# Optimization experiments

Hardware: AMD Instinct MI355X
Metric: run time of the kernel (lower is better)

## Reference

```python
import jax, jax.numpy as jnp
from jax import lax
import numpy as np

IMG = 224
NB = IMG // 8  # 28 blocks per spatial dim

# DCT-II (ortho) 8x8 basis matrix
_D = np.cos(np.pi * (2 * np.arange(8)[None, :] + 1) * np.arange(8)[:, None] / 16.0) * np.sqrt(2.0 / 8.0)
_D[0, :] *= 1.0 / np.sqrt(2.0)
DCT8 = jnp.asarray(_D, dtype=jnp.float32)


def _conv(x, w, b, s):
    y = lax.conv_general_dilated(x, w, (s, s), 'SAME', dimension_numbers=('NCHW', 'OIHW', 'NCHW'))
    return y + b[None, :, None, None]


def _pool7(h):  # adaptive avg pool 56x56 -> 7x7, flatten
    B = h.shape[0]
    return h.reshape(B, 64, 7, 8, 7, 8).mean(axis=(3, 5)).reshape(B, -1)


def setup_inputs() -> dict:
    key = jax.random.key(0)
    ks = jax.random.split(key, 16)
    r = jax.nn.initializers.normal(0.02)
    inp = {
        'x': jax.random.uniform(ks[0], (64, 3, IMG, IMG), jnp.float32),
        'w_stem': r(ks[1], (64, 3, 7, 7), jnp.float32), 'b_stem': jnp.zeros((64,), jnp.float32),
        'w1': r(ks[2], (128, 64, 3, 3), jnp.float32), 'b1': jnp.zeros((128,), jnp.float32),
        'w2': r(ks[3], (256, 128, 3, 3), jnp.float32), 'b2': jnp.zeros((256,), jnp.float32),
        'w3': r(ks[4], (512, 256, 3, 3), jnp.float32), 'b3': jnp.zeros((512,), jnp.float32),
        'wd1': r(ks[5], (32, 3, 3, 3), jnp.float32), 'bd1': jnp.zeros((32,), jnp.float32),
        'wd2': r(ks[6], (64, 32, 3, 3), jnp.float32), 'bd2': jnp.zeros((64,), jnp.float32),
        'wf1': r(ks[7], (32, 6, 3, 3), jnp.float32), 'bf1': jnp.zeros((32,), jnp.float32),
        'wf2': r(ks[8], (64, 32, 3, 3), jnp.float32), 'bf2': jnp.zeros((64,), jnp.float32),
        'W_freq': r(ks[9], (6272, 512), jnp.float32), 'b_freq': jnp.zeros((512,), jnp.float32),
        'W_fu1': r(ks[10], (1024, 1024), jnp.float32), 'b_fu1': jnp.zeros((1024,), jnp.float32),
        'W_fu2': r(ks[11], (1024, 512), jnp.float32), 'b_fu2': jnp.zeros((512,), jnp.float32),
        'W_cls': r(ks[12], (512, 2), jnp.float32), 'b_cls': jnp.zeros((2,), jnp.float32),
        'temp': 1.5 * jnp.ones((1,), jnp.float32),
    }
    return inp


def reference(x, w_stem, b_stem, w1, b1, w2, b2, w3, b3, wd1, bd1, wd2, bd2,
              wf1, bf1, wf2, bf2, W_freq, b_freq, W_fu1, b_fu1, W_fu2, b_fu2,
              W_cls, b_cls, temp):
    relu = jax.nn.relu
    B = x.shape[0]
    # --- CNN backbone (resnet18 surrogate): 4 stride-2 stages -> GAP 512 ---
    h = relu(_conv(x, w_stem, b_stem, 2))
    h = relu(_conv(h, w1, b1, 2))
    h = relu(_conv(h, w2, b2, 2))
    h = relu(_conv(h, w3, b3, 2))
    backbone_feat = h.mean(axis=(2, 3))  # [B, 512]
    # --- DCT branch: grayscale -> batched 8x8 block DCT-II ortho -> mean -> resize ---
    gray = (0.299 * x[:, 0] + 0.587 * x[:, 1] + 0.114 * x[:, 2]) * 255.0  # [B,224,224]
    blocks = gray.reshape(B, NB, 8, NB, 8).transpose(0, 1, 3, 2, 4)  # [B,28,28,8,8]
    dctb = jnp.einsum('ij,bmnjk,lk->bmnil', DCT8, blocks, DCT8)  # D @ blk @ D^T
    dct_img = dctb.mean(axis=(1, 2))  # [B,8,8]
    dct_img = jax.image.resize(dct_img, (B, IMG, IMG), 'bilinear')
    dct_in = jnp.broadcast_to(dct_img[:, None], (B, 3, IMG, IMG))
    hd = relu(_conv(dct_in, wd1, bd1, 2))
    hd = relu(_conv(hd, wd2, bd2, 2))  # [B,64,56,56]
    dct_pooled = _pool7(hd)  # [B,3136]
    # --- FFT branch: batched 2D FFT, interleaved real/imag per channel -> 6 ch ---
    f = jnp.fft.fft2(x)  # [B,3,224,224] complex
    fft_in = jnp.stack([f.real, f.imag], axis=2).reshape(B, 6, IMG, IMG).astype(x.dtype)
    hf = relu(_conv(fft_in, wf1, bf1, 2))
    hf = relu(_conv(hf, wf2, bf2, 2))
    fft_pooled = _pool7(hf)  # [B,3136]
    # --- fusion + classifier + temperature scaling ---
    freq = relu(jnp.concatenate([dct_pooled, fft_pooled], axis=1) @ W_freq + b_freq)
    comb = jnp.concatenate([backbone_feat, freq], axis=1)  # [B,1024]
    fused = relu(relu(comb @ W_fu1 + b_fu1) @ W_fu2 + b_fu2)
    logits = fused @ W_cls + b_cls
    calibrated = logits / temp
    return (logits, calibrated)
```

## Files before the change

kernel.cpp:

```cpp
#include <hip/hip_runtime.h>

#ifndef M_PI
#define M_PI 3.14159265358979323846
#endif


#define BATCH 64

typedef __bf16 bf16x8 __attribute__((ext_vector_type(8)));
typedef float f32x4 __attribute__((ext_vector_type(4)));

__device__ __forceinline__ unsigned short f2bf(float f) {
    unsigned u = __float_as_uint(f);
    u += 0x7FFF + ((u >> 16) & 1);
    return (unsigned short)(u >> 16);
}
__device__ __forceinline__ unsigned packsplit(float v) {
    unsigned short h = f2bf(v);
    float hf = __uint_as_float(((unsigned)h) << 16);
    unsigned short l = f2bf(v - hf);
    return (((unsigned)h) << 16) | (unsigned)l;
}

union U8frag { bf16x8 v; unsigned d[4]; };

__device__ __forceinline__ void unpack8(const unsigned* p, bf16x8& hi, bf16x8& lo) {
    uint4 a = *(const uint4*)p;
    uint4 b = *(const uint4*)(p + 4);
    U8frag H, L;
    H.d[0] = __builtin_amdgcn_perm(a.y, a.x, 0x07060302u);
    L.d[0] = __builtin_amdgcn_perm(a.y, a.x, 0x05040100u);
    H.d[1] = __builtin_amdgcn_perm(a.w, a.z, 0x07060302u);
    L.d[1] = __builtin_amdgcn_perm(a.w, a.z, 0x05040100u);
    H.d[2] = __builtin_amdgcn_perm(b.y, b.x, 0x07060302u);
    L.d[2] = __builtin_amdgcn_perm(b.y, b.x, 0x05040100u);
    H.d[3] = __builtin_amdgcn_perm(b.w, b.z, 0x07060302u);
    L.d[3] = __builtin_amdgcn_perm(b.w, b.z, 0x05040100u);
    hi = H.v; lo = L.v;
}

__device__ __forceinline__ bf16x8 bfneg(bf16x8 v) {
    U8frag a; a.v = v;
    a.d[0] ^= 0x80008000u; a.d[1] ^= 0x80008000u;
    a.d[2] ^= 0x80008000u; a.d[3] ^= 0x80008000u;
    return a.v;
}

__global__ void prep_w(const float* __restrict__ w, unsigned* __restrict__ dst,
                       int Co, int Ci) {
    int idx = blockIdx.x * 256 + threadIdx.x;
    int tot = Co * Ci * 9;
    if (idx >= tot) return;
    int k9 = idx % 9;
    int rest = idx / 9;
    int ci = rest % Ci, co = rest / Ci;
    dst[((size_t)k9 * Co + co) * Ci + ci] = packsplit(w[idx]);
}

__global__ void pack_f32(const float* __restrict__ src, unsigned* __restrict__ dst, int n) {
    int i = blockIdx.x * 256 + threadIdx.x;
    if (i < n) dst[i] = packsplit(src[i]);
}

__global__ __launch_bounds__(256)
void conv3x3s2_mfma(const unsigned* __restrict__ inP, const unsigned* __restrict__ wP,
                    const float* __restrict__ bias,
                    unsigned* __restrict__ outPk, float* __restrict__ outF0,
                    float* __restrict__ outF1,
                    int Ci, int Co, int Hin, int Win, int Hout, int Wout,
                    int NTOT, int ciPer, int mode) {
    __shared__ unsigned sA[128 * 36];
    __shared__ unsigned sB[64 * 36];
    const int tid = threadIdx.x;
    const int wv = tid >> 6, lane = tid & 63;
    const int ciBeg = blockIdx.z * ciPer;
    const int coT0 = blockIdx.y * 128;
    const int HWin = Hin * Win, HWout = Hout * Wout;

    const int nG = blockIdx.x * 64 + (tid >> 2);
    const int kqB = tid & 3;
    int bb = 0, yy = 0, xx = 0;
    bool nval = nG < NTOT;
    if (nval) {
        bb = nG / HWout;
        int rem = nG - bb * HWout;
        yy = rem / Wout;
        xx = rem - yy * Wout;
    }
    const unsigned baseImg = (unsigned)bb * Ci * HWin;
    const int coA = tid >> 1, halfA = tid & 1;

    f32x4 acc[2][4];
#pragma unroll
    for (int s = 0; s < 2; s++)
#pragma unroll
        for (int t = 0; t < 4; t++) acc[s][t] = (f32x4){0.f, 0.f, 0.f, 0.f};

    for (int k9 = 0; k9 < 9; k9++) {
        int ky = k9 / 3, kx = k9 - ky * 3;
        int iy = 2 * yy + ky, ix = 2 * xx + kx;
        bool bval = nval && iy < Hin && ix < Win;
        unsigned off0 = baseImg + (unsigned)iy * Win + (unsigned)ix;
        const unsigned* wbase = wP + ((size_t)k9 * Co + coT0 + coA) * Ci + ciBeg + halfA * 16;

        for (int c0 = 0; c0 < ciPer; c0 += 32) {
            __syncthreads();
            {
                const uint4* g = (const uint4*)(wbase + c0);
                uint4 v0 = g[0], v1 = g[1], v2 = g[2], v3 = g[3];
                uint4* d = (uint4*)(sA + coA * 36 + halfA * 16);
                d[0] = v0; d[1] = v1; d[2] = v2; d[3] = v3;
            }
            {
                unsigned u[8];
                const unsigned cbase = off0 + (unsigned)(ciBeg + c0 + kqB * 8) * HWin;
#pragma unroll
                for (int j = 0; j < 8; j++)
                    u[j] = bval ? inP[cbase + (unsigned)j * HWin] : 0u;
                uint4* d = (uint4*)(sB + (tid >> 2) * 36 + kqB * 8);
                uint4 w0; w0.x = u[0]; w0.y = u[1]; w0.z = u[2]; w0.w = u[3];
                uint4 w1; w1.x = u[4]; w1.y = u[5]; w1.z = u[6]; w1.w = u[7];
                d[0] = w0; d[1] = w1;
            }
            __syncthreads();

            bf16x8 ah[2], al[2], bh[4], bl[4];
            const int m = lane & 15, q = lane >> 4;
#pragma unroll
            for (int s = 0; s < 2; s++)
                unpack8(sA + (wv * 32 + s * 16 + m) * 36 + q * 8, ah[s], al[s]);
#pragma unroll
            for (int t = 0; t < 4; t++)
                unpack8(sB + (t * 16 + m) * 36 + q * 8, bh[t], bl[t]);

#pragma unroll
            for (int s = 0; s < 2; s++)
#pragma unroll
                for (int t = 0; t < 4; t++)
                    acc[s][t] = __builtin_amdgcn_mfma_f32_16x16x32_bf16(ah[s], bh[t], acc[s][t], 0, 0, 0);
#pragma unroll
            for (int s = 0; s < 2; s++)
#pragma unroll
                for (int t = 0; t < 4; t++)
                    acc[s][t] = __builtin_amdgcn_mfma_f32_16x16x32_bf16(ah[s], bl[t], acc[s][t], 0, 0, 0);
#pragma unroll
            for (int s = 0; s < 2; s++)
#pragma unroll
                for (int t = 0; t < 4; t++)
                    acc[s][t] = __builtin_amdgcn_mfma_f32_16x16x32_bf16(al[s], bh[t], acc[s][t], 0, 0, 0);
        }
    }

    const int m = lane & 15, q = lane >> 4;
#pragma unroll
    for (int t = 0; t < 4; t++) {
        int n_g = blockIdx.x * 64 + t * 16 + m;
        if (n_g >= NTOT) continue;
        int b = n_g / HWout;
        int rem = n_g - b * HWout;
        size_t nb = (size_t)b * Co * HWout + rem;
#pragma unroll
        for (int s = 0; s < 2; s++) {
            int co_l = wv * 32 + s * 16 + q * 4;
#pragma unroll
            for (int r = 0; r < 4; r++) {
                int co_g = coT0 + co_l + r;
                float v = acc[s][t][r];
                size_t addr = nb + (size_t)co_g * HWout;
                if (mode == 0) {
                    v += bias[co_g];
                    v = v > 0.f ? v : 0.f;
                    outPk[addr] = packsplit(v);
                } else {
                    (blockIdx.z == 0 ? outF0 : outF1)[addr] = v;
                }
            }
        }
    }
}

__global__ __launch_bounds__(256)
void conv3x3s2_mfma64(const unsigned* __restrict__ inP, const unsigned* __restrict__ wP,
                      const float* __restrict__ bias, float* __restrict__ outF,
                      int Hin, int Win, int Hout, int Wout, int NTOT) {
    const int Ci = 32;
    __shared__ unsigned sA[64 * 36];
    __shared__ unsigned sB[64 * 36];
    const int tid = threadIdx.x;
    const int wv = tid >> 6, lane = tid & 63;
    const int HWin = Hin * Win, HWout = Hout * Wout;

    const int nG = blockIdx.x * 64 + (tid >> 2);
    const int kq = tid & 3;
    int bb = 0, yy = 0, xx = 0;
    bool nval = nG < NTOT;
    if (nval) {
        bb = nG / HWout;
        int rem = nG - bb * HWout;
        yy = rem / Wout;
        xx = rem - yy * Wout;
    }
    const unsigned baseImg = (unsigned)bb * Ci * HWin;
    const int ch = wv & 1, nh = wv >> 1;

    f32x4 acc[2][2];
#pragma unroll
    for (int s = 0; s < 2; s++)
#pragma unroll
        for (int t = 0; t < 2; t++) acc[s][t] = (f32x4){0.f, 0.f, 0.f, 0.f};

    for (int k9 = 0; k9 < 9; k9++) {
        int ky = k9 / 3, kx = k9 - ky * 3;
        int iy = 2 * yy + ky, ix = 2 * xx + kx;
        bool bval = nval && iy < Hin && ix < Win;
        unsigned off0 = baseImg + (unsigned)iy * Win + (unsigned)ix;
        __syncthreads();
        {
            const unsigned* g = wP + ((size_t)k9 * 64 + (tid >> 2)) * Ci + kq * 8;
            uint4 v0 = *(const uint4*)g;
            uint4 v1 = *(const uint4*)(g + 4);
            uint4* d = (uint4*)(sA + (tid >> 2) * 36 + kq * 8);
            d[0] = v0; d[1] = v1;
        }
        {
            unsigned u[8];
            const unsigned cbase = off0 + (unsigned)(kq * 8) * HWin;
#pragma unroll
            for (int j = 0; j < 8; j++)
                u[j] = bval ? inP[cbase + (unsigned)j * HWin] : 0u;
            uint4* d = (uint4*)(sB + (tid >> 2) * 36 + kq * 8);
            uint4 w0; w0.x = u[0]; w0.y = u[1]; w0.z = u[2]; w0.w = u[3];
            uint4 w1; w1.x = u[4]; w1.y = u[5]; w1.z = u[6]; w1.w = u[7];
            d[0] = w0; d[1] = w1;
        }
        __syncthreads();

        bf16x8 ah[2], al[2], bh[2], bl[2];
        const int m = lane & 15, q = lane >> 4;
#pragma unroll
        for (int s = 0; s < 2; s++)
            unpack8(sA + (ch * 32 + s * 16 + m) * 36 + q * 8, ah[s], al[s]);
#pragma unroll
        for (int t = 0; t < 2; t++)
            unpack8(sB + (nh * 32 + t * 16 + m) * 36 + q * 8, bh[t], bl[t]);

#pragma unroll
        for (int s = 0; s < 2; s++)
#pragma unroll
            for (int t = 0; t < 2; t++)
                acc[s][t] = __builtin_amdgcn_mfma_f32_16x16x32_bf16(ah[s], bh[t], acc[s][t], 0, 0, 0);
#pragma unroll
        for (int s = 0; s < 2; s++)
#pragma unroll
            for (int t = 0; t < 2; t++)
                acc[s][t] = __builtin_amdgcn_mfma_f32_16x16x32_bf16(ah[s], bl[t], acc[s][t], 0, 0, 0);
#pragma unroll
        for (int s = 0; s < 2; s++)
#pragma unroll
            for (int t = 0; t < 2; t++)
                acc[s][t] = __builtin_amdgcn_mfma_f32_16x16x32_bf16(al[s], bh[t], acc[s][t], 0, 0, 0);
    }

    const int m = lane & 15, q = lane >> 4;
#pragma unroll
    for (int t = 0; t < 2; t++) {
        int n_g = blockIdx.x * 64 + nh * 32 + t * 16 + m;
        if (n_g >= NTOT) continue;
        int b = n_g / HWout;
        int rem = n_g - b * HWout;
        size_t nb = (size_t)b * 64 * HWout + rem;
#pragma unroll
        for (int s = 0; s < 2; s++) {
            int co0 = ch * 32 + s * 16 + q * 4;
#pragma unroll
            for (int r = 0; r < 4; r++) {
                int co = co0 + r;
                float v = acc[s][t][r] + bias[co];
                outF[nb + (size_t)co * HWout] = v > 0.f ? v : 0.f;
            }
        }
    }
}

__global__ void make_dft(unsigned* __restrict__ wre, unsigned* __restrict__ wim) {
    int idx = blockIdx.x * 256 + threadIdx.x;
    if (idx >= 224 * 224) return;
    int j = idx / 224, k = idx % 224;
    int m = (j * k) % 224;
    double a = -2.0 * M_PI * (double)m / 224.0;
    wre[idx] = packsplit((float)cos(a));
    wim[idx] = packsplit((float)sin(a));
}

__global__ void make_wsum(const float* __restrict__ wd1, float* __restrict__ wsum) {
    int idx = threadIdx.x;
    if (idx >= 288) return;
    int o = idx / 9, k = idx % 9;
    wsum[idx] = wd1[o * 27 + k] + wd1[o * 27 + 9 + k] + wd1[o * 27 + 18 + k];
}

__global__ __launch_bounds__(64)
void dft_mfma_s1(const unsigned* __restrict__ wre, const unsigned* __restrict__ wim,
                 const unsigned* __restrict__ xpk,
                 unsigned* __restrict__ ttre, unsigned* __restrict__ ttim) {
    const int z = blockIdx.z;
    const int m0 = blockIdx.x * 32, n0 = blockIdx.y * 32;
    const int lane = threadIdx.x;
    const int ml = lane & 15, q = lane >> 4;
    const unsigned* xb = xpk + (size_t)z * 50176;

    f32x4 cre[2][2], cim[2][2];
#pragma unroll
    for (int s = 0; s < 2; s++)
#pragma unroll
        for (int t = 0; t < 2; t++) { cre[s][t] = (f32x4){0,0,0,0}; cim[s][t] = (f32x4){0,0,0,0}; }

    for (int k0 = 0; k0 < 224; k0 += 32) {
        bf16x8 arh[2], arl[2], aih[2], ail[2], bh[2], bl[2];
#pragma unroll
        for (int s = 0; s < 2; s++) {
            int row = m0 + s * 16 + ml;
            unpack8(wre + row * 224 + k0 + q * 8, arh[s], arl[s]);
            unpack8(wim + row * 224 + k0 + q * 8, aih[s], ail[s]);
        }
#pragma unroll
        for (int t = 0; t < 2; t++)
            unpack8(xb + (n0 + t * 16 + ml) * 224 + k0 + q * 8, bh[t], bl[t]);

#pragma unroll
        for (int s = 0; s < 2; s++)
#pragma unroll
            for (int t = 0; t < 2; t++) {
                cre[s][t] = __builtin_amdgcn_mfma_f32_16x16x32_bf16(arh[s], bh[t], cre[s][t], 0, 0, 0);
                cre[s][t] = __builtin_amdgcn_mfma_f32_16x16x32_bf16(arh[s], bl[t], cre[s][t], 0, 0, 0);
                cre[s][t] = __builtin_amdgcn_mfma_f32_16x16x32_bf16(arl[s], bh[t], cre[s][t], 0, 0, 0);
                cim[s][t] = __builtin_amdgcn_mfma_f32_16x16x32_bf16(aih[s], bh[t], cim[s][t], 0, 0, 0);
                cim[s][t] = __builtin_amdgcn_mfma_f32_16x16x32_bf16(aih[s], bl[t], cim[s][t], 0, 0, 0);
                cim[s][t] = __builtin_amdgcn_mfma_f32_16x16x32_bf16(ail[s], bh[t], cim[s][t], 0, 0, 0);
            }
    }

    unsigned* tre = ttre + (size_t)z * 50176;
    unsigned* tim = ttim + (size_t)z * 50176;
#pragma unroll
    for (int s = 0; s < 2; s++)
#pragma unroll
        for (int t = 0; t < 2; t++)
#pragma unroll
            for (int r = 0; r < 4; r++) {
                int m = m0 + s * 16 + q * 4 + r;
                int n = n0 + t * 16 + ml;
                tre[m * 224 + n] = packsplit(cre[s][t][r]);
                tim[m * 224 + n] = packsplit(cim[s][t][r]);
            }
}

__global__ __launch_bounds__(64)
void dft_mfma_s2(const unsigned* __restrict__ wre, const unsigned* __restrict__ wim,
                 const unsigned* __restrict__ ttre, const unsigned* __restrict__ ttim,
                 float* __restrict__ fft_in) {
    const int z = blockIdx.z;
    const int m0 = blockIdx.x * 32, n0 = blockIdx.y * 32;
    const int lane = threadIdx.x;
    const int ml = lane & 15, q = lane >> 4;
    const unsigned* tre = ttre + (size_t)z * 50176;
    const unsigned* tim = ttim + (size_t)z * 50176;

    f32x4 cre[2][2], cim[2][2];
#pragma unroll
    for (int s = 0; s < 2; s++)
#pragma unroll
        for (int t = 0; t < 2; t++) { cre[s][t] = (f32x4){0,0,0,0}; cim[s][t] = (f32x4){0,0,0,0}; }

    for (int k0 = 0; k0 < 224; k0 += 32) {
        bf16x8 arh[2], arl[2], aih[2], ail[2];
        bf16x8 brh[2], brl[2], bih[2], bil[2];
#pragma unroll
        for (int s = 0; s < 2; s++) {
            int row = m0 + s * 16 + ml;
            unpack8(wre + row * 224 + k0 + q * 8, arh[s], arl[s]);
            unpack8(wim + row * 224 + k0 + q * 8, aih[s], ail[s]);
        }
#pragma unroll
        for (int t = 0; t < 2; t++) {
            int row = n0 + t * 16 + ml;
            unpack8(tre + row * 224 + k0 + q * 8, brh[t], brl[t]);
            unpack8(tim + row * 224 + k0 + q * 8, bih[t], bil[t]);
        }

#pragma unroll
        for (int t = 0; t < 2; t++) {
            bf16x8 nih = bfneg(bih[t]);
            bf16x8 nil = bfneg(bil[t]);
#pragma unroll
            for (int s = 0; s < 2; s++) {
                cre[s][t] = __builtin_amdgcn_mfma_f32_16x16x32_bf16(arh[s], brh[t], cre[s][t], 0, 0, 0);
                cre[s][t] = __builtin_amdgcn_mfma_f32_16x16x32_bf16(arh[s], brl[t], cre[s][t], 0, 0, 0);
                cre[s][t] = __builtin_amdgcn_mfma_f32_16x16x32_bf16(arl[s], brh[t], cre[s][t], 0, 0, 0);
                cre[s][t] = __builtin_amdgcn_mfma_f32_16x16x32_bf16(aih[s], nih, cre[s][t], 0, 0, 0);
                cre[s][t] = __builtin_amdgcn_mfma_f32_16x16x32_bf16(aih[s], nil, cre[s][t], 0, 0, 0);
                cre[s][t] = __builtin_amdgcn_mfma_f32_16x16x32_bf16(ail[s], nih, cre[s][t], 0, 0, 0);
                cim[s][t] = __builtin_amdgcn_mfma_f32_16x16x32_bf16(arh[s], bih[t], cim[s][t], 0, 0, 0);
                cim[s][t] = __builtin_amdgcn_mfma_f32_16x16x32_bf16(arh[s], bil[t], cim[s][t], 0, 0, 0);
                cim[s][t] = __builtin_amdgcn_mfma_f32_16x16x32_bf16(arl[s], bih[t], cim[s][t], 0, 0, 0);
                cim[s][t] = __builtin_amdgcn_mfma_f32_16x16x32_bf16(aih[s], brh[t], cim[s][t], 0, 0, 0);
                cim[s][t] = __builtin_amdgcn_mfma_f32_16x16x32_bf16(aih[s], brl[t], cim[s][t], 0, 0, 0);
                cim[s][t] = __builtin_amdgcn_mfma_f32_16x16x32_bf16(ail[s], brh[t], cim[s][t], 0, 0, 0);
            }
        }
    }

    const int b_loc = z / 3, c = z % 3;
    float* yre = fft_in + (size_t)(b_loc * 6 + 2 * c) * 50176;
    float* yim = yre + 50176;
#pragma unroll
    for (int s = 0; s < 2; s++)
#pragma unroll
        for (int t = 0; t < 2; t++)
#pragma unroll
            for (int r = 0; r < 4; r++) {
                int m = m0 + s * 16 + q * 4 + r;
                int n = n0 + t * 16 + ml;
                yre[m * 224 + n] = cre[s][t][r];
                yim[m * 224 + n] = cim[s][t][r];
            }
}

template <int CO_BLK, int TH, int TW, int CI_CHUNK, bool PACK>
__global__ __launch_bounds__(CO_BLK * TH)
void conv3x3_s2(const float* __restrict__ in, const float* __restrict__ w,
                const float* __restrict__ bias, float* __restrict__ out,
                int Ci, int Co, int Hin, int Win, int Hout, int Wout) {
    constexpr int IN_H = 2 * TH + 1;
    constexpr int IN_W = 2 * TW + 1;
    constexpr int IN_WP = 32;
    constexpr int WSTR = (CI_CHUNK * 9) | 1;
    __shared__ __align__(16) float s_in[CI_CHUNK][IN_H][IN_WP];
    __shared__ float s_w[CO_BLK * WSTR];

    const int tid = threadIdx.x;
    const int tiles_x = Wout / TW;
    const int tile = blockIdx.x;
    const int ty0 = (tile / tiles_x) * TH;
    const int tx0 = (tile % tiles_x) * TW;
    const int cog = blockIdx.y;
    const int b = blockIdx.z;
    const int co = tid % CO_BLK;
    const int ty = tid / CO_BLK;
    const int co_g = cog * CO_BLK + co;

    float acc[TW];
#pragma unroll
    for (int i = 0; i < TW; i++) acc[i] = 0.f;

    const float* in_b = in + (size_t)b * Ci * Hin * Win;
    const int iy0 = 2 * ty0, ix0 = 2 * tx0;

    for (int ci0 = 0; ci0 < Ci; ci0 += CI_CHUNK) {
        for (int idx = tid; idx < CI_CHUNK * IN_H * IN_W; idx += CO_BLK * TH) {
            int ci = idx / (IN_H * IN_W);
            int rem = idx % (IN_H * IN_W);
            int r = rem / IN_W, cc = rem % IN_W;
            int gy = iy0 + r, gx = ix0 + cc;
            float v = 0.f;
            if (gy < Hin && gx < Win)
                v = in_b[(size_t)(ci0 + ci) * Hin * Win + (size_t)gy * Win + gx];
            s_in[ci][r][cc] = v;
        }
        for (int idx = tid; idx < CO_BLK * CI_CHUNK * 9; idx += CO_BLK * TH) {
            int c = idx / (CI_CHUNK * 9);
            int k = idx % (CI_CHUNK * 9);
            s_w[c * WSTR + k] = w[((size_t)(cog * CO_BLK + c) * Ci + ci0) * 9 + k];
        }
        __syncthreads();

#pragma unroll
        for (int ci = 0; ci < CI_CHUNK; ci++) {
            float wr[9];
#pragma unroll
            for (int k = 0; k < 9; k++) wr[k] = s_w[co * WSTR + ci * 9 + k];
#pragma unroll
            for (int ky = 0; ky < 3; ky++) {
                float r[IN_WP];
                const float4* rowp = (const float4*)&s_in[ci][2 * ty + ky][0];
#pragma unroll
                for (int qq = 0; qq < IN_WP / 4; qq++) {
                    float4 v = rowp[qq];
                    r[4 * qq] = v.x; r[4 * qq + 1] = v.y; r[4 * qq + 2] = v.z; r[4 * qq + 3] = v.w;
                }
#pragma unroll
                for (int kx = 0; kx < 3; kx++) {
                    float wv = wr[ky * 3 + kx];
#pragma unroll
                    for (int xq = 0; xq < TW; xq++) acc[xq] += r[2 * xq + kx] * wv;
                }
            }
        }
        __syncthreads();
    }
    float bb = bias[co_g];
    size_t obase = ((size_t)b * Co + co_g) * Hout * Wout + (size_t)(ty0 + ty) * Wout + tx0;
#pragma unroll
    for (int xq = 0; xq < TW; xq++) {
        float v = acc[xq] + bb;
        v = v > 0.f ? v : 0.f;
        if (PACK)
            ((unsigned*)out)[obase + xq] = packsplit(v);
        else
            out[obase + xq] = v;
    }
}

__global__ __launch_bounds__(256)
void conv7x7_s2_pack(const float* __restrict__ in, const float* __restrict__ w,
                     const float* __restrict__ bias, unsigned* __restrict__ out) {
    constexpr int TH = 4, TW = 14;
    constexpr int IN_H = 13, IN_W = 33, IN_WP = 36, WSTR = 149;
    __shared__ __align__(16) float s_in[3][IN_H][IN_WP];
    __shared__ float s_w[64 * WSTR];
    const int tid = threadIdx.x;
    const int tile = blockIdx.x;
    const int tiles_x = 112 / TW;
    const int ty0 = (tile / tiles_x) * TH;
    const int tx0 = (tile % tiles_x) * TW;
    const int b = blockIdx.z;
    const int co = tid & 63;
    const int ty = tid >> 6;

    const float* in_b = in + (size_t)b * 3 * 224 * 224;
    const int iy0 = 2 * ty0 - 2, ix0 = 2 * tx0 - 2;

    for (int idx = tid; idx < 3 * IN_H * IN_W; idx += 256) {
        int ci = idx / (IN_H * IN_W);
        int rem = idx % (IN_H * IN_W);
        int r = rem / IN_W, cc = rem % IN_W;
        int gy = iy0 + r, gx = ix0 + cc;
        float v = 0.f;
        if (gy >= 0 && gy < 224 && gx >= 0 && gx < 224)
            v = in_b[(size_t)ci * 224 * 224 + (size_t)gy * 224 + gx];
        s_in[ci][r][cc] = v;
    }
    for (int idx = tid; idx < 64 * 147; idx += 256) {
        int c = idx / 147, k = idx % 147;
        s_w[c * WSTR + k] = w[c * 147 + k];
    }
    __syncthreads();

    float acc[TW];
#pragma unroll
    for (int i = 0; i < TW; i++) acc[i] = 0.f;

#pragma unroll
    for (int ci = 0; ci < 3; ci++) {
#pragma unroll
        for (int ky = 0; ky < 7; ky++) {
            float wr[7];
#pragma unroll
            for (int k = 0; k < 7; k++) wr[k] = s_w[co * WSTR + ci * 49 + ky * 7 + k];
            float r[IN_WP];
            const float4* rowp = (const float4*)&s_in[ci][2 * ty + ky][0];
#pragma unroll
            for (int qq = 0; qq < IN_WP / 4; qq++) {
                float4 v = rowp[qq];
                r[4 * qq] = v.x; r[4 * qq + 1] = v.y; r[4 * qq + 2] = v.z; r[4 * qq + 3] = v.w;
            }
#pragma unroll
            for (int kx = 0; kx < 7; kx++) {
                float wv = wr[kx];
#pragma unroll
                for (int xq = 0; xq < TW; xq++) acc[xq] += r[2 * xq + kx] * wv;
            }
        }
    }
    float bb = bias[co];
    unsigned* outp = out + ((size_t)b * 64 + co) * 112 * 112 + (size_t)(ty0 + ty) * 112 + tx0;
#pragma unroll
    for (int xq = 0; xq < TW; xq++) {
        float v = acc[xq] + bb;
        v = v > 0.f ? v : 0.f;
        outp[xq] = packsplit(v);
    }
}

__device__ __forceinline__ float dct_coef(int u, int i) {
    if (u == 0) return 0.35355339059327373f;
    return 0.5f * cosf((float)M_PI * (float)((2 * i + 1) * u) / 16.0f);
}

__global__ __launch_bounds__(256)
void dct_partial(const float* __restrict__ x, float* __restrict__ accum) {
    __shared__ float red[256];
    const int b = blockIdx.x, g = blockIdx.y;
    const int tid = threadIdx.x;
    const int ij = tid & 63;
    const int grp = tid >> 6;
    const int i = ij >> 3, j = ij & 7;
    const float* xb = x + (size_t)b * 3 * 50176;
    float s = 0.f;
    for (int blk = g * 4 + grp; blk < 784; blk += 48) {
        int m = blk / 28, n = blk % 28;
        size_t o = (size_t)(m * 8 + i) * 224 + n * 8 + j;
        s += 0.299f * xb[o] + 0.587f * xb[50176 + o] + 0.114f * xb[2 * 50176 + o];
    }
    red[tid] = s;
    __syncthreads();
    if (tid < 64)
        atomicAdd(&accum[b * 64 + tid],
                  red[tid] + red[tid + 64] + red[tid + 128] + red[tid + 192]);
}

__global__ __launch_bounds__(64)
void dct_final(const float* __restrict__ accum, float* __restrict__ dct_out) {
    __shared__ float Mb[64];
    const int b = blockIdx.x, tid = threadIdx.x;
    Mb[tid] = accum[b * 64 + tid] * (255.f / 784.f);
    __syncthreads();
    int u = tid >> 3, v = tid & 7;
    float acc = 0.f;
#pragma unroll
    for (int i2 = 0; i2 < 8; i2++) {
        float du = dct_coef(u, i2);
#pragma unroll
        for (int j2 = 0; j2 < 8; j2++) acc += du * Mb[i2 * 8 + j2] * dct_coef(v, j2);
    }
    dct_out[b * 64 + tid] = acc;
}

__global__ void resize_bilinear(const float* __restrict__ dct, float* __restrict__ out) {
    int idx = blockIdx.x * 256 + threadIdx.x;
    if (idx >= BATCH * 224 * 224) return;
    int b = idx / (224 * 224);
    int rem = idx % (224 * 224);
    int y = rem / 224, xx = rem % 224;
    float sy = fminf(fmaxf((y + 0.5f) * (1.f / 28.f) - 0.5f, 0.f), 7.f);
    float sx = fminf(fmaxf((xx + 0.5f) * (1.f / 28.f) - 0.5f, 0.f), 7.f);
    int y0 = (int)floorf(sy); if (y0 > 6) y0 = 6;
    int x0 = (int)floorf(sx); if (x0 > 6) x0 = 6;
    float ty = sy - y0, tx = sx - x0;
    const float* M = dct + b * 64;
    float v00 = M[y0 * 8 + x0], v01 = M[y0 * 8 + x0 + 1];
    float v10 = M[(y0 + 1) * 8 + x0], v11 = M[(y0 + 1) * 8 + x0 + 1];
    out[idx] = (1.f - ty) * ((1.f - tx) * v00 + tx * v01) + ty * ((1.f - tx) * v10 + tx * v11);
}

__global__ void pool7(const float* __restrict__ h, float* __restrict__ out,
                      int col_base, int n) {
    int idx = blockIdx.x * 256 + threadIdx.x;
    if (idx >= n) return;
    int b = idx / (64 * 49);
    int rem = idx % (64 * 49);
    int c = rem / 49;
    int ij = rem % 49;
    int i = ij / 7, j = ij % 7;
    const float* hp = h + ((size_t)(b * 64 + c)) * 56 * 56 + (size_t)i * 8 * 56 + j * 8;
    float s = 0.f;
#pragma unroll
    for (int r = 0; r < 8; r++)
#pragma unroll
        for (int q = 0; q < 8; q++) s += hp[r * 56 + q];
    out[(size_t)b * 6272 + col_base + c * 49 + ij] = s * (1.f / 64.f);
}

__global__ void gap2_kernel(const float* __restrict__ ha, const float* __restrict__ hb,
                            const float* __restrict__ bias, float* __restrict__ comb,
                            int nwaves) {
    int gt = blockIdx.x * blockDim.x + threadIdx.x;
    int wid = gt >> 6;
    int lane = gt & 63;
    if (wid >= nwaves) return;
    int b = wid / 512, c = wid % 512;
    const float* pa = ha + (size_t)wid * 196;
    const float* pb = hb + (size_t)wid * 196;
    float bbv = bias[c];
    float s = 0.f;
    for (int i = lane; i < 196; i += 64) {
        float v = pa[i] + pb[i] + bbv;
        s += v > 0.f ? v : 0.f;
    }
#pragma unroll
    for (int off = 32; off > 0; off >>= 1) s += __shfl_down(s, off);
    if (lane == 0) comb[(size_t)b * 1024 + c] = s * (1.f / 196.f);
}

__global__ __launch_bounds__(256)
void gemm64_atomic(const float* __restrict__ A, const float* __restrict__ Bm,
                   float* __restrict__ C, int N, int K, int KC) {
    __shared__ __align__(16) float sA[16][68];
    __shared__ __align__(16) float sB[16][68];
    const int tid = threadIdx.x;
    const int n0 = blockIdx.x * 64;
    const int kbase = blockIdx.z * KC;
    const int tr = (tid >> 4) << 2;
    const int tc = (tid & 15) << 2;
    float acc[4][4];
#pragma unroll
    for (int r = 0; r < 4; r++)
#pragma unroll
        for (int c = 0; c < 4; c++) acc[r][c] = 0.f;

    for (int k0 = 0; k0 < KC; k0 += 16) {
        for (int i = tid; i < 1024; i += 256) {
            int m = i >> 4, k = i & 15;
            sA[k][m] = A[(size_t)m * K + kbase + k0 + k];
        }
        for (int i = tid; i < 1024; i += 256) {
            int k = i >> 6, n = i & 63;
            sB[k][n] = Bm[(size_t)(kbase + k0 + k) * N + n0 + n];
        }
        __syncthreads();
#pragma unroll
        for (int k = 0; k < 16; k++) {
            float4 a = *(const float4*)&sA[k][tr];
            float4 bv = *(const float4*)&sB[k][tc];
            float av[4] = {a.x, a.y, a.z, a.w};
            float bb[4] = {bv.x, bv.y, bv.z, bv.w};
#pragma unroll
            for (int r = 0; r < 4; r++)
#pragma unroll
                for (int c = 0; c < 4; c++) acc[r][c] += av[r] * bb[c];
        }
        __syncthreads();
    }
#pragma unroll
    for (int r = 0; r < 4; r++)
#pragma unroll
        for (int c = 0; c < 4; c++)
            atomicAdd(&C[(size_t)(tr + r) * N + n0 + tc + c], acc[r][c]);
}

__global__ void bias_relu_copy(const float* __restrict__ src, const float* __restrict__ bias,
                               float* __restrict__ dst, int N, int dstStride, int dstOff) {
    int idx = blockIdx.x * 256 + threadIdx.x;
    if (idx >= BATCH * N) return;
    int b = idx / N, n = idx % N;
    float v = src[idx] + bias[n];
    dst[(size_t)b * dstStride + dstOff + n] = v > 0.f ? v : 0.f;
}

__global__ void logits_kernel(const float* __restrict__ fused, const float* __restrict__ Wc,
                              const float* __restrict__ bcls, const float* __restrict__ temp,
                              float* __restrict__ out) {
    int idx = threadIdx.x;
    if (idx >= 128) return;
    int b = idx >> 1, n = idx & 1;
    float s = bcls[n];
    const float* f = fused + (size_t)b * 512;
    for (int k = 0; k < 512; k++) s += f[k] * Wc[k * 2 + n];
    out[idx] = s;
    out[128 + idx] = s / temp[0];
}

extern "C" void kernel_launch(void* const* d_in, const int* in_sizes, int n_in,
                              void* d_out, int out_size, void* d_ws, size_t ws_size,
                              hipStream_t stream) {
    const float* x      = (const float*)d_in[0];
    const float* w_stem = (const float*)d_in[1];
    const float* b_stem = (const float*)d_in[2];
    const float* w1 = (const float*)d_in[3];   const float* b1 = (const float*)d_in[4];
    const float* w2 = (const float*)d_in[5];   const float* b2 = (const float*)d_in[6];
    const float* w3 = (const float*)d_in[7];   const float* b3 = (const float*)d_in[8];
    const float* wd1 = (const float*)d_in[9];  const float* bd1 = (const float*)d_in[10];
    const float* wd2 = (const float*)d_in[11]; const float* bd2 = (const float*)d_in[12];
    const float* wf1 = (const float*)d_in[13]; const float* bf1 = (const float*)d_in[14];
    const float* wf2 = (const float*)d_in[15]; const float* bf2 = (const float*)d_in[16];
    const float* W_freq = (const float*)d_in[17]; const float* b_freq = (const float*)d_in[18];
    const float* W_fu1  = (const float*)d_in[19]; const float* b_fu1  = (const float*)d_in[20];
    const float* W_fu2  = (const float*)d_in[21]; const float* b_fu2  = (const float*)d_in[22];
    const float* W_cls  = (const float*)d_in[23]; const float* b_cls  = (const float*)d_in[24];
    const float* temp   = (const float*)d_in[25];
    float* ws = (float*)d_ws;
    float* out = (float*)d_out;

    const size_t IMG2 = 224 * 224;

    size_t oWRE  = 0;
    size_t oWIM  = oWRE + IMG2;
    size_t oWSUM = oWIM + IMG2;
    size_t oDCT  = oWSUM + 288;
    size_t oDIMG = oDCT + (size_t)BATCH * 64;
    size_t oFREQIN  = oDIMG + (size_t)BATCH * IMG2;
    size_t oCOMB    = oFREQIN + (size_t)BATCH * 6272;
    size_t oFREQACC = oCOMB + (size_t)BATCH * 1024;
    size_t oFU1     = oFREQACC + (size_t)BATCH * 512;
    size_t oFUSED   = oFU1 + (size_t)BATCH * 1024;
    size_t oDCTACC  = oFUSED + (size_t)BATCH * 512;
    size_t oW1s     = oDCTACC + (size_t)BATCH * 64;
    size_t oW2s     = oW1s + 73728;
    size_t oW3s     = oW2s + 294912;
    size_t oWF2s    = oW3s + 1179648;
    size_t oWD2s    = oWF2s + 18432;
    size_t P        = oWD2s + 18432;

    int CB = 16;
    while (CB > 1 && (P + (size_t)CB * 1605632) * 4 > ws_size) CB >>= 1;
    size_t base   = P;
    size_t oSTEMP = base;
    size_t oC1P   = oSTEMP + (size_t)CB * 802816;
    size_t oC2P   = oC1P + (size_t)CB * 401408;
    size_t oC3a   = oC2P + (size_t)CB * 200704;
    size_t oC3b   = oC3a + (size_t)CB * 100352;
    size_t oXPK   = base;
    size_t oTTRE  = oXPK + (size_t)CB * 150528;
    size_t oTTIM  = oTTRE + (size_t)CB * 150528;
    size_t oFFTIN = oTTIM + (size_t)CB * 150528;
    size_t oBIG1  = oC1P;
    size_t oBIG2  = oC2P;

    unsigned* WREp = (unsigned*)(ws + oWRE);
    unsigned* WIMp = (unsigned*)(ws + oWIM);
    unsigned* W1s = (unsigned*)(ws + oW1s);
    unsigned* W2s = (unsigned*)(ws + oW2s);
    unsigned* W3s = (unsigned*)(ws + oW3s);
    unsigned* WF2s = (unsigned*)(ws + oWF2s);
    unsigned* WD2s = (unsigned*)(ws + oWD2s);
    unsigned* STEMP = (unsigned*)(ws + oSTEMP);
    unsigned* C1P   = (unsigned*)(ws + oC1P);
    unsigned* C2P   = (unsigned*)(ws + oC2P);
    unsigned* XPK   = (unsigned*)(ws + oXPK);
    unsigned* TTRE  = (unsigned*)(ws + oTTRE);
    unsigned* TTIM  = (unsigned*)(ws + oTTIM);
    unsigned* BIG1P = (unsigned*)(ws + oBIG1);

    hipMemsetAsync(ws + oFREQACC, 0,
                   (size_t)BATCH * (512 + 1024 + 512 + 64) * sizeof(float), stream);
    make_dft<<<196, 256, 0, stream>>>(WREp, WIMp);
    make_wsum<<<1, 288, 0, stream>>>(wd1, ws + oWSUM);
    prep_w<<<(128 * 64 * 9 + 255) / 256, 256, 0, stream>>>(w1, W1s, 128, 64);
    prep_w<<<(256 * 128 * 9 + 255) / 256, 256, 0, stream>>>(w2, W2s, 256, 128);
    prep_w<<<(512 * 256 * 9 + 255) / 256, 256, 0, stream>>>(w3, W3s, 512, 256);
    prep_w<<<(64 * 32 * 9 + 255) / 256, 256, 0, stream>>>(wf2, WF2s, 64, 32);
    prep_w<<<(64 * 32 * 9 + 255) / 256, 256, 0, stream>>>(wd2, WD2s, 64, 32);
    dct_partial<<<dim3(BATCH, 12), 256, 0, stream>>>(x, ws + oDCTACC);
    dct_final<<<BATCH, 64, 0, stream>>>(ws + oDCTACC, ws + oDCT);
    resize_bilinear<<<12544, 256, 0, stream>>>(ws + oDCT, ws + oDIMG);

    for (int b0 = 0; b0 < BATCH; b0 += CB) {
        const float* xc = x + (size_t)b0 * 3 * IMG2;
        pack_f32<<<(CB * 3 * (int)IMG2 + 255) / 256, 256, 0, stream>>>(
            xc, XPK, CB * 3 * (int)IMG2);
        dft_mfma_s1<<<dim3(7, 7, 3 * CB), 64, 0, stream>>>(WREp, WIMp, XPK, TTRE, TTIM);
        dft_mfma_s2<<<dim3(7, 7, 3 * CB), 64, 0, stream>>>(WREp, WIMp, TTRE, TTIM, ws + oFFTIN);
        conv3x3_s2<32, 8, 14, 6, true><<<dim3(112, 1, CB), 256, 0, stream>>>(
            ws + oFFTIN, wf1, bf1, ws + oBIG1, 6, 32, 224, 224, 112, 112);
        conv3x3s2_mfma64<<<dim3(CB * 3136 / 64, 1, 1), 256, 0, stream>>>(
            BIG1P, WF2s, bf2, ws + oBIG2, 112, 112, 56, 56, CB * 3136);
        pool7<<<(CB * 64 * 49 + 255) / 256, 256, 0, stream>>>(
            ws + oBIG2, ws + oFREQIN + (size_t)b0 * 6272, 3136, CB * 64 * 49);
        conv3x3_s2<32, 8, 14, 1, true><<<dim3(112, 1, CB), 256, 0, stream>>>(
            ws + oDIMG + (size_t)b0 * IMG2, ws + oWSUM, bd1, ws + oBIG1, 1, 32, 224, 224, 112, 112);
        conv3x3s2_mfma64<<<dim3(CB * 3136 / 64, 1, 1), 256, 0, stream>>>(
            BIG1P, WD2s, bd2, ws + oBIG2, 112, 112, 56, 56, CB * 3136);
        pool7<<<(CB * 64 * 49 + 255) / 256, 256, 0, stream>>>(
            ws + oBIG2, ws + oFREQIN + (size_t)b0 * 6272, 0, CB * 64 * 49);
        conv7x7_s2_pack<<<dim3(224, 1, CB), 256, 0, stream>>>(xc, w_stem, b_stem, STEMP);
        conv3x3s2_mfma<<<dim3((CB * 3136 + 63) / 64, 1, 1), 256, 0, stream>>>(
            STEMP, W1s, b1, C1P, nullptr, nullptr,
            64, 128, 112, 112, 56, 56, CB * 3136, 64, 0);
        conv3x3s2_mfma<<<dim3((CB * 784 + 63) / 64, 2, 1), 256, 0, stream>>>(
            C1P, W2s, b2, C2P, nullptr, nullptr,
            128, 256, 56, 56, 28, 28, CB * 784, 128, 0);
        conv3x3s2_mfma<<<dim3((CB * 196 + 63) / 64, 4, 2), 256, 0, stream>>>(
            C2P, W3s, b3, nullptr, ws + oC3a, ws + oC3b,
            256, 512, 28, 28, 14, 14, CB * 196, 128, 1);
        gap2_kernel<<<(CB * 512 * 64 + 255) / 256, 256, 0, stream>>>(
            ws + oC3a, ws + oC3b, b3, ws + oCOMB + (size_t)b0 * 1024, CB * 512);
    }

    gemm64_atomic<<<dim3(8, 1, 98), 256, 0, stream>>>(ws + oFREQIN, W_freq, ws + oFREQACC,
                                                      512, 6272, 64);
    bias_relu_copy<<<128, 256, 0, stream>>>(ws + oFREQACC, b_freq, ws + oCOMB, 512, 1024, 512);
    gemm64_atomic<<<dim3(16, 1, 16), 256, 0, stream>>>(ws + oCOMB, W_fu1, ws + oFU1,
                                                       1024, 1024, 64);
    bias_relu_copy<<<256, 256, 0, stream>>>(ws + oFU1, b_fu1, ws + oFU1, 1024, 1024, 0);
    gemm64_atomic<<<dim3(8, 1, 16), 256, 0, stream>>>(ws + oFU1, W_fu2, ws + oFUSED,
                                                      512, 1024, 64);
    bias_relu_copy<<<128, 256, 0, stream>>>(ws + oFUSED, b_fu2, ws + oFUSED, 512, 512, 0);
    logits_kernel<<<1, 128, 0, stream>>>(ws + oFUSED, W_cls, b_cls, temp, out);
}
```

Before: 2.192 ms.

## Run 7x7 stem conv as split-bf16 MFMA implicit GEMM on packed input

Replaces the scalar FP32 7x7 stride-2 stem convolution with an implicit-GEMM kernel on bf16 MFMA, using hi/lo split operands (three MFMAs per step) to keep near-FP32 accuracy. It reuses the already-packed input XPK from the FFT path, and a new prep kernel lays out the stem weights with K padded to 224 (ci padded to 4, kx to 8). The workspace is reshuffled so XPK stays alive until the stem runs, aliasing the FFT temporaries and C3 buffers onto other regions. The padding wastes MFMA work, and the input gather reads scattered global memory without shared-memory reuse.

```diff
diff --git a/kernel.cpp b/kernel.cpp
--- a/kernel.cpp
+++ b/kernel.cpp
@@ -55,6 +55,17 @@
     int rest = idx / 9;
     int ci = rest % Ci, co = rest / Ci;
     dst[((size_t)k9 * Co + co) * Ci + ci] = packsplit(w[idx]);
+}
+
+__global__ void prep_wstem(const float* __restrict__ w, unsigned* __restrict__ dst) {
+    int idx = blockIdx.x * 256 + threadIdx.x;
+    if (idx >= 64 * 224) return;
+    int co = idx / 224, k = idx % 224;
+    int ci = k & 3, kx = (k >> 2) & 7, ky = k >> 5;
+    float v = 0.f;
+    if (ci < 3 && kx < 7)
+        v = w[((co * 3 + ci) * 7 + ky) * 7 + kx];
+    dst[idx] = packsplit(v);
 }
 
 __global__ void pack_f32(const float* __restrict__ src, unsigned* __restrict__ dst, int n) {
@@ -282,6 +293,115 @@
     }
 }
 
+__global__ __launch_bounds__(256)
+void conv7x7s2_mfma(const unsigned* __restrict__ inP, const unsigned* __restrict__ wP,
+                    const float* __restrict__ bias, unsigned* __restrict__ outPk,
+                    int NTOT) {
+    __shared__ unsigned sA[64 * 36];
+    __shared__ unsigned sB[64 * 36];
+    const int tid = threadIdx.x;
+    const int wv = tid >> 6, lane = tid & 63;
+    const int HWout = 112 * 112;
+
+    const int nG = blockIdx.x * 64 + (tid >> 2);
+    const int kq = tid & 3;
+    bool nval = nG < NTOT;
+    int bb = 0, yy = 0, xx = 0;
+    if (nval) {
+        bb = nG / HWout;
+        int rem = nG - bb * HWout;
+        yy = rem / 112;
+        xx = rem - yy * 112;
+    }
+    const int iy0 = 2 * yy - 2, ix0 = 2 * xx - 2;
+    const unsigned baseImg = (unsigned)bb * 3 * 50176;
+    const int ch = wv & 1, nh = wv >> 1;
+
+    f32x4 acc[2][2];
+#pragma unroll
+    for (int s = 0; s < 2; s++)
+#pragma unroll
+        for (int t = 0; t < 2; t++) acc[s][t] = (f32x4){0.f, 0.f, 0.f, 0.f};
+
+#pragma unroll
+    for (int kyc = 0; kyc < 7; kyc++) {
+        const int c0 = kyc * 32;
+        const int iy = iy0 + kyc;
+        const bool iyv = nval && iy >= 0 && iy < 224;
+        __syncthreads();
+        {
+            const unsigned* g = wP + (tid >> 2) * 224 + c0 + kq * 8;
+            uint4 v0 = *(const uint4*)g;
+            uint4 v1 = *(const uint4*)(g + 4);
+            uint4* d = (uint4*)(sA + (tid >> 2) * 36 + kq * 8);
+            d[0] = v0; d[1] = v1;
+        }
+        {
+            unsigned u[8];
+            const unsigned rowbase = baseImg + (unsigned)(iy * 224);
+#pragma unroll
+            for (int j = 0; j < 8; j++) {
+                int ci = j & 3;
+                int kx = kq * 2 + (j >> 2);
+                int ix = ix0 + kx;
+                bool v = iyv && ci < 3 && kx < 7 && ix >= 0 && ix < 224;
+                u[j] = v ? inP[rowbase + (unsigned)(ci * 50176 + ix)] : 0u;
+            }
+            uint4* d = (uint4*)(sB + (tid >> 2) * 36 + kq * 8);
+            uint4 w0; w0.x = u[0]; w0.y = u[1]; w0.z = u[2]; w0.w = u[3];
+            uint4 w1; w1.x = u[4]; w1.y = u[5]; w1.z = u[6]; w1.w = u[7];
+            d[0] = w0; d[1] = w1;
+        }
+        __syncthreads();
+
+        bf16x8 ah[2], al[2], bh[2], bl[2];
+        const int m = lane & 15, q = lane >> 4;
+#pragma unroll
+        for (int s = 0; s < 2; s++)
+            unpack8(sA + (ch * 32 + s * 16 + m) * 36 + q * 8, ah[s], al[s]);
+#pragma unroll
+        for (int t = 0; t < 2; t++)
+            unpack8(sB + (nh * 32 + t * 16 + m) * 36 + q * 8, bh[t], bl[t]);
+
+#pragma unroll
+        for (int s = 0; s < 2; s++)
+#pragma unroll
+            for (int t = 0; t < 2; t++)
+                acc[s][t] = __builtin_amdgcn_mfma_f32_16x16x32_bf16(ah[s], bh[t], acc[s][t], 0, 0, 0);
+#pragma unroll
+        for (int s = 0; s < 2; s++)
+#pragma unroll
+            for (int t = 0; t < 2; t++)
+                acc[s][t] = __builtin_amdgcn_mfma_f32_16x16x32_bf16(ah[s], bl[t], acc[s][t], 0, 0, 0);
+#pragma unroll
+        for (int s = 0; s < 2; s++)
+#pragma unroll
+            for (int t = 0; t < 2; t++)
+                acc[s][t] = __builtin_amdgcn_mfma_f32_16x16x32_bf16(al[s], bh[t], acc[s][t], 0, 0, 0);
+    }
+
+    const int m = lane & 15, q = lane >> 4;
+#pragma unroll
+    for (int t = 0; t < 2; t++) {
+        int n_g = blockIdx.x * 64 + nh * 32 + t * 16 + m;
+        if (n_g >= NTOT) continue;
+        int b = n_g / HWout;
+        int rem = n_g - b * HWout;
+        size_t nb = (size_t)b * 64 * HWout + rem;
+#pragma unroll
+        for (int s = 0; s < 2; s++) {
+            int co0 = ch * 32 + s * 16 + q * 4;
+#pragma unroll
+            for (int r = 0; r < 4; r++) {
+                int co = co0 + r;
+                float v = acc[s][t][r] + bias[co];
+                v = v > 0.f ? v : 0.f;
+                outPk[nb + (size_t)co * HWout] = packsplit(v);
+            }
+        }
+    }
+}
+
 __global__ void make_dft(unsigned* __restrict__ wre, unsigned* __restrict__ wim) {
     int idx = blockIdx.x * 256 + threadIdx.x;
     if (idx >= 224 * 224) return;
@@ -508,77 +628,6 @@
             ((unsigned*)out)[obase + xq] = packsplit(v);
         else
             out[obase + xq] = v;
-    }
-}
-
-__global__ __launch_bounds__(256)
-void conv7x7_s2_pack(const float* __restrict__ in, const float* __restrict__ w,
-                     const float* __restrict__ bias, unsigned* __restrict__ out) {
-    constexpr int TH = 4, TW = 14;
-    constexpr int IN_H = 13, IN_W = 33, IN_WP = 36, WSTR = 149;
-    __shared__ __align__(16) float s_in[3][IN_H][IN_WP];
-    __shared__ float s_w[64 * WSTR];
-    const int tid = threadIdx.x;
-    const int tile = blockIdx.x;
-    const int tiles_x = 112 / TW;
-    const int ty0 = (tile / tiles_x) * TH;
-    const int tx0 = (tile % tiles_x) * TW;
-    const int b = blockIdx.z;
-    const int co = tid & 63;
-    const int ty = tid >> 6;
-
-    const float* in_b = in + (size_t)b * 3 * 224 * 224;
-    const int iy0 = 2 * ty0 - 2, ix0 = 2 * tx0 - 2;
-
-    for (int idx = tid; idx < 3 * IN_H * IN_W; idx += 256) {
-        int ci = idx / (IN_H * IN_W);
-        int rem = idx % (IN_H * IN_W);
-        int r = rem / IN_W, cc = rem % IN_W;
-        int gy = iy0 + r, gx = ix0 + cc;
-        float v = 0.f;
-        if (gy >= 0 && gy < 224 && gx >= 0 && gx < 224)
-            v = in_b[(size_t)ci * 224 * 224 + (size_t)gy * 224 + gx];
-        s_in[ci][r][cc] = v;
-    }
-    for (int idx = tid; idx < 64 * 147; idx += 256) {
-        int c = idx / 147, k = idx % 147;
-        s_w[c * WSTR + k] = w[c * 147 + k];
-    }
-    __syncthreads();
-
-    float acc[TW];
-#pragma unroll
-    for (int i = 0; i < TW; i++) acc[i] = 0.f;
-
-#pragma unroll
-    for (int ci = 0; ci < 3; ci++) {
-#pragma unroll
-        for (int ky = 0; ky < 7; ky++) {
-            float wr[7];
-#pragma unroll
-            for (int k = 0; k < 7; k++) wr[k] = s_w[co * WSTR + ci * 49 + ky * 7 + k];
-            float r[IN_WP];
-            const float4* rowp = (const float4*)&s_in[ci][2 * ty + ky][0];
-#pragma unroll
-            for (int qq = 0; qq < IN_WP / 4; qq++) {
-                float4 v = rowp[qq];
-                r[4 * qq] = v.x; r[4 * qq + 1] = v.y; r[4 * qq + 2] = v.z; r[4 * qq + 3] = v.w;
-            }
-#pragma unroll
-            for (int kx = 0; kx < 7; kx++) {
-                float wv = wr[kx];
-#pragma unroll
-                for (int xq = 0; xq < TW; xq++) acc[xq] += r[2 * xq + kx] * wv;
-            }
-        }
-    }
-    float bb = bias[co];
-    unsigned* outp = out + ((size_t)b * 64 + co) * 112 * 112 + (size_t)(ty0 + ty) * 112 + tx0;
-#pragma unroll
-    for (int xq = 0; xq < TW; xq++) {
-        float v = acc[xq] + bb;
-        v = v > 0.f ? v : 0.f;
-        outp[xq] = packsplit(v);
     }
 }
 
@@ -789,20 +838,21 @@
     size_t oW3s     = oW2s + 294912;
     size_t oWF2s    = oW3s + 1179648;
     size_t oWD2s    = oWF2s + 18432;
-    size_t P        = oWD2s + 18432;
+    size_t oWSTEMs  = oWD2s + 18432;
+    size_t P        = oWSTEMs + 14336;
 
     int CB = 16;
     while (CB > 1 && (P + (size_t)CB * 1605632) * 4 > ws_size) CB >>= 1;
     size_t base   = P;
-    size_t oSTEMP = base;
+    size_t oXPK   = base;
+    size_t oSTEMP = base + (size_t)CB * 150528;
     size_t oC1P   = oSTEMP + (size_t)CB * 802816;
     size_t oC2P   = oC1P + (size_t)CB * 401408;
-    size_t oC3a   = oC2P + (size_t)CB * 200704;
-    size_t oC3b   = oC3a + (size_t)CB * 100352;
-    size_t oXPK   = base;
-    size_t oTTRE  = oXPK + (size_t)CB * 150528;
-    size_t oTTIM  = oTTRE + (size_t)CB * 150528;
-    size_t oFFTIN = oTTIM + (size_t)CB * 150528;
+    size_t oC3a   = base;
+    size_t oC3b   = base + (size_t)CB * 100352;
+    size_t oTTRE  = oSTEMP;
+    size_t oTTIM  = oSTEMP + (size_t)CB * 150528;
+    size_t oFFTIN = oSTEMP + (size_t)CB * 301056;
     size_t oBIG1  = oC1P;
     size_t oBIG2  = oC2P;
 
@@ -813,6 +863,7 @@
     unsigned* W3s = (unsigned*)(ws + oW3s);
     unsigned* WF2s = (unsigned*)(ws + oWF2s);
     unsigned* WD2s = (unsigned*)(ws + oWD2s);
+    unsigned* WSTEMs = (unsigned*)(ws + oWSTEMs);
     unsigned* STEMP = (unsigned*)(ws + oSTEMP);
     unsigned* C1P   = (unsigned*)(ws + oC1P);
     unsigned* C2P   = (unsigned*)(ws + oC2P);
@@ -830,6 +881,7 @@
     prep_w<<<(512 * 256 * 9 + 255) / 256, 256, 0, stream>>>(w3, W3s, 512, 256);
     prep_w<<<(64 * 32 * 9 + 255) / 256, 256, 0, stream>>>(wf2, WF2s, 64, 32);
     prep_w<<<(64 * 32 * 9 + 255) / 256, 256, 0, stream>>>(wd2, WD2s, 64, 32);
+    prep_wstem<<<(64 * 224 + 255) / 256, 256, 0, stream>>>(w_stem, WSTEMs);
     dct_partial<<<dim3(BATCH, 12), 256, 0, stream>>>(x, ws + oDCTACC);
     dct_final<<<BATCH, 64, 0, stream>>>(ws + oDCTACC, ws + oDCT);
     resize_bilinear<<<12544, 256, 0, stream>>>(ws + oDCT, ws + oDIMG);
@@ -852,7 +904,8 @@
             BIG1P, WD2s, bd2, ws + oBIG2, 112, 112, 56, 56, CB * 3136);
         pool7<<<(CB * 64 * 49 + 255) / 256, 256, 0, stream>>>(
             ws + oBIG2, ws + oFREQIN + (size_t)b0 * 6272, 0, CB * 64 * 49);
-        conv7x7_s2_pack<<<dim3(224, 1, CB), 256, 0, stream>>>(xc, w_stem, b_stem, STEMP);
+        conv7x7s2_mfma<<<dim3(CB * 196, 1, 1), 256, 0, stream>>>(
+            XPK, WSTEMs, b_stem, STEMP, CB * 12544);
         conv3x3s2_mfma<<<dim3((CB * 3136 + 63) / 64, 1, 1), 256, 0, stream>>>(
             STEMP, W1s, b1, C1P, nullptr, nullptr,
             64, 128, 112, 112, 56, 56, CB * 3136, 64, 0);
```

After: 2.077 ms. 5.2% less time.
